# Kernel optimization log

Measured on AMD Instinct MI355X. Metric: run time of the kernel, lower is better.

## Reference

```python
import jax, jax.numpy as jnp
import numpy as np


def _hat(w):
    wx, wy, wz = w[..., 0], w[..., 1], w[..., 2]
    O = jnp.zeros_like(wx)
    return jnp.stack([
        jnp.stack([O, -wz, wy], -1),
        jnp.stack([wz, O, -wx], -1),
        jnp.stack([-wy, wx, O], -1)], -2)


def so3_exp_map(w):
    # w: [B,3] axis-angle -> [B,3,3] rotation (Rodrigues with Taylor fallback)
    th2 = jnp.sum(w * w, -1)[..., None, None]
    th = jnp.sqrt(th2 + 1e-30)
    a = jnp.where(th2 > 1e-8, jnp.sin(th) / th, 1.0 - th2 / 6.0)
    b = jnp.where(th2 > 1e-8, (1.0 - jnp.cos(th)) / th2, 0.5 - th2 / 24.0)
    K = _hat(w)
    I = jnp.eye(3, dtype=w.dtype)
    return I + a * K + b * (K @ K)


def _trilinear(vol, pts):
    # vol: [X,Y,Z]; pts: [N,3] voxel coords; zero outside the volume
    dims = jnp.asarray(vol.shape, dtype=pts.dtype)
    inside = jnp.all((pts >= 0.0) & (pts <= dims - 1.0), axis=-1)
    p0 = jnp.floor(pts)
    f = pts - p0
    hi = jnp.asarray(vol.shape, dtype=jnp.int32) - 1
    i0 = jnp.clip(p0.astype(jnp.int32), 0, hi)
    i1 = jnp.clip(i0 + 1, 0, hi)
    x0, y0, z0 = i0[:, 0], i0[:, 1], i0[:, 2]
    x1, y1, z1 = i1[:, 0], i1[:, 1], i1[:, 2]
    fx, fy, fz = f[:, 0], f[:, 1], f[:, 2]
    gx, gy, gz = 1.0 - fx, 1.0 - fy, 1.0 - fz
    val = (vol[x0, y0, z0] * gx * gy * gz + vol[x1, y0, z0] * fx * gy * gz
           + vol[x0, y1, z0] * gx * fy * gz + vol[x0, y0, z1] * gx * gy * fz
           + vol[x1, y1, z0] * fx * fy * gz + vol[x1, y0, z1] * fx * gy * fz
           + vol[x0, y1, z1] * gx * fy * fz + vol[x1, y1, z1] * fx * fy * fz)
    return jnp.where(inside, val, 0.0)


def setup_inputs() -> dict:
    key = jax.random.key(0)
    k1, k2, k3 = jax.random.split(key, 3)
    D = 256
    volume = jax.random.uniform(k1, (D, D, D), dtype=jnp.float32)
    spacing = jnp.ones(3, dtype=jnp.float32)                    # 1 mm voxels
    origin = jnp.full((3,), -(D - 1) / 2.0, dtype=jnp.float32)  # volume centered at 0
    isocenter = jnp.zeros(3, dtype=jnp.float32)
    sdd = jnp.array([1020.0], dtype=jnp.float32)
    # cam-to-world: source 510 mm behind isocenter on -z axis
    rt_inv = jnp.eye(4, dtype=jnp.float32).at[2, 3].set(-510.0)[None]
    # intrinsics: 512x512 detector, 2 mm pixels -> focal = sdd/pixel = 510
    f = 510.0
    K = jnp.array([[f, 0.0, 256.0], [0.0, f, 256.0], [0.0, 0.0, 1.0]], jnp.float32)
    k_inv = jnp.linalg.inv(K)
    eps = 1e-8
    rot = eps * jax.random.normal(k2, (1, 3), dtype=jnp.float32)
    xyz = eps * jax.random.normal(k3, (1, 3), dtype=jnp.float32)
    return {"volume": volume, "rt_inv": rt_inv, "k_inv": k_inv, "sdd": sdd,
            "isocenter": isocenter, "origin": origin, "spacing": spacing,
            "rot": rot, "xyz": xyz, "height": 512, "width": 512, "n_steps": 256}


def reference(volume, rt_inv, k_inv, sdd, isocenter, origin, spacing, rot, xyz,
              height, width, n_steps):
    dtype = volume.dtype
    # --- pose property: pivot @ exp(rot),R@xyz @ pivot_inv, then rt_inv @ pose ---
    R = so3_exp_map(rot)[0]                       # [3,3]
    t = R @ xyz[0]                                # einsum('bij,bj->bi')
    T = jnp.eye(4, dtype=dtype).at[:3, :3].set(R).at[:3, 3].set(t)
    rtm = rt_inv[0]
    c = (jnp.linalg.inv(rtm) @ jnp.append(isocenter, jnp.ones(1, dtype)))[:3]
    piv = jnp.eye(4, dtype=dtype).at[:3, 3].set(c)
    piv_inv = jnp.eye(4, dtype=dtype).at[:3, 3].set(-c)
    pose = rtm @ (piv @ (T @ piv_inv))            # cam-to-world, [4,4]
    # --- render: ray-march DRR ---
    u = jnp.arange(width, dtype=dtype) + 0.5
    v = jnp.arange(height, dtype=dtype) + 0.5
    uu, vv = jnp.meshgrid(u, v, indexing='xy')    # [H,W]
    pix = jnp.stack([uu.ravel(), vv.ravel(), jnp.ones(height * width, dtype)], -1)
    dir_cam = (pix @ k_inv.T) * sdd[0]            # detector points at depth sdd, cam frame
    Rw, src = pose[:3, :3], pose[:3, 3]
    dirs = dir_cam @ Rw.T                         # world-frame source->detector rays [N,3]
    seglen = jnp.linalg.norm(dirs, axis=-1) / n_steps

    def step(acc, i):
        frac = (i.astype(dtype) + 0.5) / n_steps
        pts = src + dirs * frac                   # [N,3] world points
        vox = (pts - origin) / spacing            # voxel coords
        return acc + _trilinear(volume, vox), None

    acc, _ = jax.lax.scan(step, jnp.zeros(height * width, dtype), jnp.arange(n_steps))
    img = acc * seglen                            # line-integral approximation
    return img.reshape(1, 1, height, width)
```

## Files before the change

### kernel.cpp

```cpp
#include <hip/hip_runtime.h>
#include <hip/hip_fp16.h>

#define W 512
#define H 512
#define NSTEPS 256
#define D 256
#define DM1 255.0f
#define QUAD_WS_BYTES (256ull*256ull*256ull*8ull)

struct SetupOut {
    float Rw[9];
    float src[3];
    float kinv[9];
    float sdd;
    float org[3];
    float invsp[3];
};

__device__ __forceinline__ void mat4mul(const float* A, const float* B, float* C) {
    #pragma unroll
    for (int i = 0; i < 4; ++i)
        #pragma unroll
        for (int j = 0; j < 4; ++j) {
            float s = 0.f;
            #pragma unroll
            for (int k = 0; k < 4; ++k) s += A[i*4+k] * B[k*4+j];
            C[i*4+j] = s;
        }
}

__device__ void compute_setup(const float* rt_inv, const float* k_inv, const float* sdd,
                              const float* isocenter, const float* origin, const float* spacing,
                              const float* rot, const float* xyz, SetupOut* o) {
    float wx = rot[0], wy = rot[1], wz = rot[2];
    float th2 = wx*wx + wy*wy + wz*wz;
    float th = sqrtf(th2 + 1e-30f);
    float a, b;
    if (th2 > 1e-8f) { a = sinf(th) / th; b = (1.f - cosf(th)) / th2; }
    else             { a = 1.f - th2 / 6.f; b = 0.5f - th2 / 24.f; }
    float K[9]  = {0.f,-wz,wy,  wz,0.f,-wx,  -wy,wx,0.f};
    float K2[9];
    #pragma unroll
    for (int i = 0; i < 3; ++i)
        #pragma unroll
        for (int j = 0; j < 3; ++j) {
            float s = 0.f;
            #pragma unroll
            for (int k = 0; k < 3; ++k) s += K[i*3+k] * K[k*3+j];
            K2[i*3+j] = s;
        }
    float R[9];
    #pragma unroll
    for (int i = 0; i < 9; ++i) R[i] = ((i % 4 == 0) ? 1.f : 0.f) + a*K[i] + b*K2[i];
    float t[3];
    #pragma unroll
    for (int i = 0; i < 3; ++i)
        t[i] = R[i*3+0]*xyz[0] + R[i*3+1]*xyz[1] + R[i*3+2]*xyz[2];

    float Ainv[16];
    const float* M = rt_inv;
    if (M[12] == 0.f && M[13] == 0.f && M[14] == 0.f && M[15] == 1.f) {
        const float r00=M[0],r01=M[1],r02=M[2],  r10=M[4],r11=M[5],r12=M[6],
                    r20=M[8],r21=M[9],r22=M[10];
        const float c00 = r11*r22 - r12*r21, c01 = r02*r21 - r01*r22, c02 = r01*r12 - r02*r11;
        const float c10 = r12*r20 - r10*r22, c11 = r00*r22 - r02*r20, c12 = r02*r10 - r00*r12;
        const float c20 = r10*r21 - r11*r20, c21 = r01*r20 - r00*r21, c22 = r00*r11 - r01*r10;
        const float det = r00*c00 + r01*c10 + r02*c20;
        const float id  = 1.f / det;
        const float tx = M[3], ty = M[7], tz = M[11];
        Ainv[0]=c00*id; Ainv[1]=c01*id; Ainv[2]=c02*id;
        Ainv[4]=c10*id; Ainv[5]=c11*id; Ainv[6]=c12*id;
        Ainv[8]=c20*id; Ainv[9]=c21*id; Ainv[10]=c22*id;
        Ainv[3]  = -(Ainv[0]*tx + Ainv[1]*ty + Ainv[2]*tz);
        Ainv[7]  = -(Ainv[4]*tx + Ainv[5]*ty + Ainv[6]*tz);
        Ainv[11] = -(Ainv[8]*tx + Ainv[9]*ty + Ainv[10]*tz);
        Ainv[12]=0.f; Ainv[13]=0.f; Ainv[14]=0.f; Ainv[15]=1.f;
    } else {
        float A[16];
        #pragma unroll
        for (int i = 0; i < 16; ++i) { A[i] = rt_inv[i]; Ainv[i] = 0.f; }
        Ainv[0] = Ainv[5] = Ainv[10] = Ainv[15] = 1.f;
        for (int c = 0; c < 4; ++c) {
            int p = c; float mx = fabsf(A[c*4+c]);
            for (int r = c+1; r < 4; ++r) { float v = fabsf(A[r*4+c]); if (v > mx) { mx = v; p = r; } }
            if (p != c) {
                for (int j = 0; j < 4; ++j) {
                    float tmp = A[c*4+j];   A[c*4+j]   = A[p*4+j];   A[p*4+j]   = tmp;
                    tmp = Ainv[c*4+j];      Ainv[c*4+j] = Ainv[p*4+j]; Ainv[p*4+j] = tmp;
                }
            }
            float inv = 1.f / A[c*4+c];
            for (int j = 0; j < 4; ++j) { A[c*4+j] *= inv; Ainv[c*4+j] *= inv; }
            for (int r = 0; r < 4; ++r) if (r != c) {
                float f = A[r*4+c];
                for (int j = 0; j < 4; ++j) { A[r*4+j] -= f*A[c*4+j]; Ainv[r*4+j] -= f*Ainv[c*4+j]; }
            }
        }
    }
    float cv[3];
    #pragma unroll
    for (int i = 0; i < 3; ++i)
        cv[i] = Ainv[i*4+0]*isocenter[0] + Ainv[i*4+1]*isocenter[1]
              + Ainv[i*4+2]*isocenter[2] + Ainv[i*4+3];

    float T[16]    = {R[0],R[1],R[2],t[0],  R[3],R[4],R[5],t[1],  R[6],R[7],R[8],t[2],  0,0,0,1};
    float piv[16]  = {1,0,0, cv[0],  0,1,0, cv[1],  0,0,1, cv[2],  0,0,0,1};
    float pivi[16] = {1,0,0,-cv[0],  0,1,0,-cv[1],  0,0,1,-cv[2],  0,0,0,1};
    float M1[16], M2[16], pose[16];
    mat4mul(T, pivi, M1);
    mat4mul(piv, M1, M2);
    mat4mul(rt_inv, M2, pose);

    #pragma unroll
    for (int i = 0; i < 3; ++i) {
        #pragma unroll
        for (int j = 0; j < 3; ++j) o->Rw[i*3+j] = pose[i*4+j];
        o->src[i] = pose[i*4+3];
    }
    #pragma unroll
    for (int i = 0; i < 9; ++i) o->kinv[i] = k_inv[i];
    o->sdd = sdd[0];
    #pragma unroll
    for (int i = 0; i < 3; ++i) { o->org[i] = origin[i]; o->invsp[i] = 1.f / spacing[i]; }
}

__global__ __launch_bounds__(256) void setup_kernel2(
    const float* __restrict__ rt_inv, const float* __restrict__ k_inv,
    const float* __restrict__ sdd, const float* __restrict__ isocenter,
    const float* __restrict__ origin, const float* __restrict__ spacing,
    const float* __restrict__ rot, const float* __restrict__ xyz,
    SetupOut* __restrict__ sp, unsigned char* __restrict__ gmask)
{
    __shared__ SetupOut S;
    if (threadIdx.x == 0) {
        compute_setup(rt_inv, k_inv, sdd, isocenter, origin, spacing, rot, xyz, &S);
        *sp = S;
    }
    __syncthreads();
    if (!gmask) return;

    __shared__ unsigned char m[256];
    m[threadIdx.x] = 0;
    __syncthreads();
    {
        const int i = threadIdx.x;
        const float frac = ((float)i + 0.5f) * (1.0f / (float)NSTEPS);
        const float Az = (S.src[2] - S.org[2]) * S.invsp[2];
        float vmin = 1e30f, vmax = -1e30f;
        #pragma unroll
        for (int c = 0; c < 4; ++c) {
            const float u = (c & 1)  ? ((float)W - 0.5f) : 0.5f;
            const float v = (c >> 1) ? ((float)H - 0.5f) : 0.5f;
            const float dcx = (S.kinv[0]*u + S.kinv[1]*v + S.kinv[2]) * S.sdd;
            const float dcy = (S.kinv[3]*u + S.kinv[4]*v + S.kinv[5]) * S.sdd;
            const float dcz = (S.kinv[6]*u + S.kinv[7]*v + S.kinv[8]) * S.sdd;
            const float dz  = S.Rw[6]*dcx + S.Rw[7]*dcy + S.Rw[8]*dcz;
            const float Bz  = dz * S.invsp[2];
            const float vz  = fmaf(Bz, frac, Az);
            vmin = fminf(vmin, vz);
            vmax = fmaxf(vmax, vz);
        }
        const int zlo = max(0,     (int)floorf(vmin - 0.05f));
        const int zhi = min(D - 1, (int)floorf(vmax + 0.05f) + 1);
        for (int z = zlo; z <= zhi; ++z) m[z] = 1;
    }
    __syncthreads();
    gmask[threadIdx.x] = m[threadIdx.x];
}

__global__ __launch_bounds__(256) void repack_quad_h(const float* __restrict__ vol,
                                                     uint2* __restrict__ ws,
                                                     const unsigned char* __restrict__ gmask) {
    const int x  = blockIdx.x;
    const int y0 = blockIdx.y * 128;
    const int z0 = blockIdx.z * 64;
    const int tid  = threadIdx.x;

    __shared__ unsigned int  tf2[129 * 32];
    __shared__ unsigned short halo_h[129];
    __shared__ unsigned char zm[64];
    const int xbase = x << 16;
    const int zh = min(z0 + 64, D - 1);

    if (tid < 64) zm[tid] = gmask ? gmask[z0 + tid] : (unsigned char)1;

    {
        const int s  = tid & 31;
        const int r0 = tid >> 5;
        for (int r = r0; r <= 128; r += 8) {
            const int y = min(y0 + r, D - 1);
            const float2 f = reinterpret_cast<const float2*>(vol + xbase + (y << 8) + z0)[s];
            __half2 h = __floats2half2_rn(f.x, f.y);
            tf2[r * 32 + (s ^ (r & 31))] = *reinterpret_cast<unsigned int*>(&h);
        }
        if (tid <= 128) {
            const int y = min(y0 + tid, D - 1);
            __half hh = __float2half_rn(vol[xbase + (y << 8) + zh]);
            halo_h[tid] = *reinterpret_cast<unsigned short*>(&hh);
        }
    }
    __syncthreads();

    const int grp  = tid >> 6;
    const int lane = tid & 63;
    const int ra = 2 * lane, rb = 2 * lane + 1, rc = 2 * lane + 2;
    for (int wp = grp; wp < 32; wp += 4) {
        const bool we = zm[2 * wp] != 0;
        const bool wo = zm[2 * wp + 1] != 0;
        if (!(we | wo)) continue;
        const unsigned int a = tf2[ra * 32 + (wp ^ (ra & 31))];
        const unsigned int b = tf2[rb * 32 + (wp ^ (rb & 31))];
        const unsigned int c = tf2[rc * 32 + (wp ^ (rc & 31))];
        const int zeven = z0 + 2 * wp;
        if (we) {
            uint4 q; q.x = a; q.y = b; q.z = b; q.w = c;
            *reinterpret_cast<uint4*>(ws + xbase + (zeven << 8) + y0 + ra) = q;
        }
        if (wo) {
            unsigned int na, nb, nc;
            if (wp < 31) {
                na = tf2[ra * 32 + ((wp + 1) ^ (ra & 31))] & 0xffffu;
                nb = tf2[rb * 32 + ((wp + 1) ^ (rb & 31))] & 0xffffu;
                nc = tf2[rc * 32 + ((wp + 1) ^ (rc & 31))] & 0xffffu;
            } else {
                na = halo_h[ra]; nb = halo_h[rb]; nc = halo_h[rc];
            }
            uint4 q;
            q.x = (a >> 16) | (na << 16);
            q.y = (b >> 16) | (nb << 16);
            q.z = q.y;
            q.w = (c >> 16) | (nc << 16);
            *reinterpret_cast<uint4*>(ws + xbase + ((zeven + 1) << 8) + y0 + ra) = q;
        }
    }
}

struct RayState {
    float Ax, Ay, Az, Bx, By, Bz, seglen;
    int imin, imax;
    bool any;
};

__device__ __forceinline__ RayState ray_setup(const SetupOut* S, int ix, int iy) {
    RayState r;
    const float u = (float)ix + 0.5f;
    const float v = (float)iy + 0.5f;
    const float dcx = (S->kinv[0]*u + S->kinv[1]*v + S->kinv[2]) * S->sdd;
    const float dcy = (S->kinv[3]*u + S->kinv[4]*v + S->kinv[5]) * S->sdd;
    const float dcz = (S->kinv[6]*u + S->kinv[7]*v + S->kinv[8]) * S->sdd;
    const float dx = S->Rw[0]*dcx + S->Rw[1]*dcy + S->Rw[2]*dcz;
    const float dy = S->Rw[3]*dcx + S->Rw[4]*dcy + S->Rw[5]*dcz;
    const float dz = S->Rw[6]*dcx + S->Rw[7]*dcy + S->Rw[8]*dcz;
    r.seglen = sqrtf(dx*dx + dy*dy + dz*dz) * (1.0f / (float)NSTEPS);
    r.Ax = (S->src[0] - S->org[0]) * S->invsp[0];
    r.Ay = (S->src[1] - S->org[1]) * S->invsp[1];
    r.Az = (S->src[2] - S->org[2]) * S->invsp[2];
    r.Bx = dx * S->invsp[0];
    r.By = dy * S->invsp[1];
    r.Bz = dz * S->invsp[2];

    float fmin = 0.f, fmax = 1.f;
    bool empty = false;
    const float aa[3] = { r.Ax, r.Ay, r.Az };
    const float bb[3] = { r.Bx, r.By, r.Bz };
    #pragma unroll
    for (int k = 0; k < 3; ++k) {
        if (fabsf(bb[k]) > 1e-12f) {
            const float rcp = 1.f / bb[k];
            const float t0 = (0.f - aa[k]) * rcp;
            const float t1 = (DM1 - aa[k]) * rcp;
            fmin = fmaxf(fmin, fminf(t0, t1));
            fmax = fminf(fmax, fmaxf(t0, t1));
        } else if (aa[k] < 0.f || aa[k] > DM1) {
            empty = true;
        }
    }
    r.any = !empty && (fmax >= fmin);
    r.imin = max(0,          (int)floorf(fmin * (float)NSTEPS - 0.5f) - 1);
    r.imax = min(NSTEPS - 1, (int)ceilf (fmax * (float)NSTEPS - 0.5f) + 1);
    return r;
}

__global__ __launch_bounds__(256) void drr_quad_kernel(
    const uint2* __restrict__ wsq, const SetupOut* __restrict__ S,
    float* __restrict__ out)
{
    const int b   = blockIdx.x;
    const int xcd = b & 7;
    const int j   = b >> 3;
    const int uu  = xcd * 16 + (j & 15);
    const int vv  = j >> 4;

    const int seg = threadIdx.x & 3;
    const int iy = vv * 16 + (threadIdx.x >> 2);
    const int ix = uu * 4  + threadIdx.y;
    const RayState r = ray_setup(S, ix, iy);

    float acc = 0.f;
    if (r.any) {
        #pragma unroll 8
        for (int i = r.imin + seg; i <= r.imax; i += 4) {
            const float frac = ((float)i + 0.5f) * (1.0f / (float)NSTEPS);
            const float vx = fmaf(r.Bx, frac, r.Ax);
            const float vy = fmaf(r.By, frac, r.Ay);
            const float vz = fmaf(r.Bz, frac, r.Az);
            const bool inside = (vx >= 0.f) && (vx <= DM1) &&
                                (vy >= 0.f) && (vy <= DM1) &&
                                (vz >= 0.f) && (vz <= DM1);
            const float cx = fminf(fmaxf(vx, 0.f), DM1);
            const float cy = fminf(fmaxf(vy, 0.f), DM1);
            const float cz = fminf(fmaxf(vz, 0.f), DM1);
            const float px = floorf(cx), py = floorf(cy), pz = floorf(cz);
            const int x0 = (int)px, y0 = (int)py, z0 = (int)pz;
            const int x1 = min(x0 + 1, D - 1);
            const float fx = cx - px, fy = cy - py, fz = cz - pz;
            const float gx = 1.f - fx, gy = 1.f - fy, gz = 1.f - fz;

            const int e0 = (x0 << 16) + (z0 << 8) + y0;
            const int e1 = e0 + ((x1 - x0) << 16);

            const uint2 q0 = wsq[e0];
            const uint2 q1 = wsq[e1];
            const float2 a0 = __half22float2(*reinterpret_cast<const __half2*>(&q0.x));
            const float2 a1 = __half22float2(*reinterpret_cast<const __half2*>(&q0.y));
            const float2 b0 = __half22float2(*reinterpret_cast<const __half2*>(&q1.x));
            const float2 b1 = __half22float2(*reinterpret_cast<const __half2*>(&q1.y));

            const float c00 = a0.x*gz + a0.y*fz;
            const float c01 = a1.x*gz + a1.y*fz;
            const float c10 = b0.x*gz + b0.y*fz;
            const float c11 = b1.x*gz + b1.y*fz;
            const float samp = (c00*gy + c01*fy)*gx + (c10*gy + c11*fy)*fx;
            acc += inside ? samp : 0.f;
        }
    }
    acc += __shfl_xor(acc, 1);
    acc += __shfl_xor(acc, 2);
    if (seg == 0)
        out[iy * W + ix] = acc * r.seglen;
}

__global__ __launch_bounds__(256) void drr_direct_kernel(
    const float* __restrict__ vol,
    const float* __restrict__ rt_inv, const float* __restrict__ k_inv,
    const float* __restrict__ sdd, const float* __restrict__ isocenter,
    const float* __restrict__ origin, const float* __restrict__ spacing,
    const float* __restrict__ rot, const float* __restrict__ xyz,
    float* __restrict__ out)
{
    __shared__ SetupOut S;
    if (threadIdx.x == 0 && threadIdx.y == 0)
        compute_setup(rt_inv, k_inv, sdd, isocenter, origin, spacing, rot, xyz, &S);
    __syncthreads();

    const int seg = threadIdx.x & 1;
    const int iy = blockIdx.x * 32 + (threadIdx.x >> 1);
    const int ix = blockIdx.y * 4  + threadIdx.y;
    const RayState r = ray_setup(&S, ix, iy);

    float acc = 0.f;
    if (r.any) {
        #pragma unroll 4
        for (int i = r.imin + seg; i <= r.imax; i += 2) {
            const float frac = ((float)i + 0.5f) * (1.0f / (float)NSTEPS);
            const float vx = fmaf(r.Bx, frac, r.Ax);
            const float vy = fmaf(r.By, frac, r.Ay);
            const float vz = fmaf(r.Bz, frac, r.Az);
            const bool inside = (vx >= 0.f) && (vx <= DM1) &&
                                (vy >= 0.f) && (vy <= DM1) &&
                                (vz >= 0.f) && (vz <= DM1);
            const float cx = fminf(fmaxf(vx, 0.f), DM1);
            const float cy = fminf(fmaxf(vy, 0.f), DM1);
            const float cz = fminf(fmaxf(vz, 0.f), DM1);
            const float px = floorf(cx), py = floorf(cy), pz = floorf(cz);
            const int x0 = (int)px, y0 = (int)py, z0 = (int)pz;
            const int x1 = min(x0 + 1, D - 1);
            const int y1 = min(y0 + 1, D - 1);
            const int z1 = min(z0 + 1, D - 1);
            const float fx = cx - px, fy = cy - py, fz = cz - pz;
            const float gx = 1.f - fx, gy = 1.f - fy, gz = 1.f - fz;

            const int base = (x0 << 16) + (y0 << 8);
            const int bx = (x1 - x0) << 16;
            const int by = (y1 - y0) << 8;

            const float v000 = vol[base + z0],           v001 = vol[base + z1];
            const float v010 = vol[base + by + z0],      v011 = vol[base + by + z1];
            const float v100 = vol[base + bx + z0],      v101 = vol[base + bx + z1];
            const float v110 = vol[base + bx + by + z0], v111 = vol[base + bx + by + z1];

            const float c00 = v000*gz + v001*fz;
            const float c01 = v010*gz + v011*fz;
            const float c10 = v100*gz + v101*fz;
            const float c11 = v110*gz + v111*fz;
            const float samp = (c00*gy + c01*fy)*gx + (c10*gy + c11*fy)*fx;
            acc += inside ? samp : 0.f;
        }
    }
    acc += __shfl_xor(acc, 1);
    if (seg == 0)
        out[iy * W + ix] = acc * r.seglen;
}

extern "C" void kernel_launch(void* const* d_in, const int* in_sizes, int n_in,
                              void* d_out, int out_size, void* d_ws, size_t ws_size,
                              hipStream_t stream) {
    const float* vol      = (const float*)d_in[0];
    const float* rt_inv   = (const float*)d_in[1];
    const float* k_inv    = (const float*)d_in[2];
    const float* sdd      = (const float*)d_in[3];
    const float* iso      = (const float*)d_in[4];
    const float* origin   = (const float*)d_in[5];
    const float* spacing  = (const float*)d_in[6];
    const float* rot      = (const float*)d_in[7];
    const float* xyz      = (const float*)d_in[8];
    float* out = (float*)d_out;

    if (ws_size >= QUAD_WS_BYTES + 4096) {
        uint2* wsq = (uint2*)d_ws;
        SetupOut* sp = (SetupOut*)((char*)d_ws + QUAD_WS_BYTES);
        unsigned char* gmask = (unsigned char*)d_ws + QUAD_WS_BYTES + 512;

        setup_kernel2<<<1, 256, 0, stream>>>(rt_inv, k_inv, sdd, iso, origin,
                                             spacing, rot, xyz, sp, gmask);
        repack_quad_h<<<dim3(D, 2, 4), 256, 0, stream>>>(vol, wsq, gmask);
        drr_quad_kernel<<<dim3(4096), dim3(64, 4), 0, stream>>>(wsq, sp, out);
    } else if (ws_size >= QUAD_WS_BYTES) {
        uint2* wsq = (uint2*)d_ws;
        SetupOut* sp = (SetupOut*)((char*)d_ws + (QUAD_WS_BYTES - 128));

        repack_quad_h<<<dim3(D, 2, 4), 256, 0, stream>>>(vol, wsq, nullptr);
        setup_kernel2<<<1, 256, 0, stream>>>(rt_inv, k_inv, sdd, iso, origin,
                                             spacing, rot, xyz, sp, nullptr);
        drr_quad_kernel<<<dim3(4096), dim3(64, 4), 0, stream>>>(wsq, sp, out);
    } else {
        drr_direct_kernel<<<dim3(H / 32, W / 4), dim3(64, 4), 0, stream>>>(
            vol, rt_inv, k_inv, sdd, iso, origin, spacing, rot, xyz, out);
    }
}
```

Before: 61.50 us.

## Replace quad-packed fp16 volume with y-pair packing to halve workspace

Changes the repacked fp16 workspace so each entry stores a y-neighbour pair (4 bytes) instead of a 2x2 y/z quad (8 bytes). This halves the repack write traffic and the workspace footprint. The cost is that the ray-march kernel now issues four gathers per sample instead of two. It also removes the fallback path used when the workspace is smaller and lowers the loop unroll from 8 to 4.

```diff
diff --git a/kernel.cpp b/kernel.cpp
--- a/kernel.cpp
+++ b/kernel.cpp
@@ -6,7 +6,7 @@
 #define NSTEPS 256
 #define D 256
 #define DM1 255.0f
-#define QUAD_WS_BYTES (256ull*256ull*256ull*8ull)
+#define PAIR_WS_BYTES (256ull*256ull*256ull*4ull)
 
 struct SetupOut {
     float Rw[9];
@@ -168,19 +168,17 @@
     gmask[threadIdx.x] = m[threadIdx.x];
 }
 
-__global__ __launch_bounds__(256) void repack_quad_h(const float* __restrict__ vol,
-                                                     uint2* __restrict__ ws,
+__global__ __launch_bounds__(256) void repack_pair_t(const float* __restrict__ vol,
+                                                     unsigned int* __restrict__ ws,
                                                      const unsigned char* __restrict__ gmask) {
     const int x  = blockIdx.x;
     const int y0 = blockIdx.y * 128;
     const int z0 = blockIdx.z * 64;
     const int tid  = threadIdx.x;
 
-    __shared__ unsigned int  tf2[129 * 32];
-    __shared__ unsigned short halo_h[129];
+    __shared__ unsigned int tf2[129 * 32];
     __shared__ unsigned char zm[64];
     const int xbase = x << 16;
-    const int zh = min(z0 + 64, D - 1);
 
     if (tid < 64) zm[tid] = gmask ? gmask[z0 + tid] : (unsigned char)1;
 
@@ -193,45 +191,23 @@
             __half2 h = __floats2half2_rn(f.x, f.y);
             tf2[r * 32 + (s ^ (r & 31))] = *reinterpret_cast<unsigned int*>(&h);
         }
-        if (tid <= 128) {
-            const int y = min(y0 + tid, D - 1);
-            __half hh = __float2half_rn(vol[xbase + (y << 8) + zh]);
-            halo_h[tid] = *reinterpret_cast<unsigned short*>(&hh);
-        }
     }
     __syncthreads();
 
     const int grp  = tid >> 6;
     const int lane = tid & 63;
     const int ra = 2 * lane, rb = 2 * lane + 1, rc = 2 * lane + 2;
-    for (int wp = grp; wp < 32; wp += 4) {
-        const bool we = zm[2 * wp] != 0;
-        const bool wo = zm[2 * wp + 1] != 0;
-        if (!(we | wo)) continue;
-        const unsigned int a = tf2[ra * 32 + (wp ^ (ra & 31))];
-        const unsigned int b = tf2[rb * 32 + (wp ^ (rb & 31))];
-        const unsigned int c = tf2[rc * 32 + (wp ^ (rc & 31))];
-        const int zeven = z0 + 2 * wp;
-        if (we) {
-            uint4 q; q.x = a; q.y = b; q.z = b; q.w = c;
-            *reinterpret_cast<uint4*>(ws + xbase + (zeven << 8) + y0 + ra) = q;
-        }
-        if (wo) {
-            unsigned int na, nb, nc;
-            if (wp < 31) {
-                na = tf2[ra * 32 + ((wp + 1) ^ (ra & 31))] & 0xffffu;
-                nb = tf2[rb * 32 + ((wp + 1) ^ (rb & 31))] & 0xffffu;
-                nc = tf2[rc * 32 + ((wp + 1) ^ (rc & 31))] & 0xffffu;
-            } else {
-                na = halo_h[ra]; nb = halo_h[rb]; nc = halo_h[rc];
-            }
-            uint4 q;
-            q.x = (a >> 16) | (na << 16);
-            q.y = (b >> 16) | (nb << 16);
-            q.z = q.y;
-            q.w = (c >> 16) | (nc << 16);
-            *reinterpret_cast<uint4*>(ws + xbase + ((zeven + 1) << 8) + y0 + ra) = q;
-        }
+    for (int w = grp; w < 64; w += 4) {
+        if (!zm[w]) continue;
+        const int wp = w >> 1;
+        const int sh = (w & 1) << 4;
+        const unsigned int ha = (tf2[ra * 32 + (wp ^ (ra & 31))] >> sh) & 0xffffu;
+        const unsigned int hb = (tf2[rb * 32 + (wp ^ (rb & 31))] >> sh) & 0xffffu;
+        const unsigned int hc = (tf2[rc * 32 + (wp ^ (rc & 31))] >> sh) & 0xffffu;
+        uint2 q;
+        q.x = ha | (hb << 16);
+        q.y = hb | (hc << 16);
+        *reinterpret_cast<uint2*>(ws + xbase + ((z0 + w) << 8) + y0 + ra) = q;
     }
 }
 
@@ -281,8 +257,8 @@
     return r;
 }
 
-__global__ __launch_bounds__(256) void drr_quad_kernel(
-    const uint2* __restrict__ wsq, const SetupOut* __restrict__ S,
+__global__ __launch_bounds__(256) void drr_pair_kernel(
+    const unsigned int* __restrict__ wsp, const SetupOut* __restrict__ S,
     float* __restrict__ out)
 {
     const int b   = blockIdx.x;
@@ -298,7 +274,7 @@
 
     float acc = 0.f;
     if (r.any) {
-        #pragma unroll 8
+        #pragma unroll 4
         for (int i = r.imin + seg; i <= r.imax; i += 4) {
             const float frac = ((float)i + 0.5f) * (1.0f / (float)NSTEPS);
             const float vx = fmaf(r.Bx, frac, r.Ax);
@@ -313,24 +289,31 @@
             const float px = floorf(cx), py = floorf(cy), pz = floorf(cz);
             const int x0 = (int)px, y0 = (int)py, z0 = (int)pz;
             const int x1 = min(x0 + 1, D - 1);
+            const int z1 = min(z0 + 1, D - 1);
             const float fx = cx - px, fy = cy - py, fz = cz - pz;
             const float gx = 1.f - fx, gy = 1.f - fy, gz = 1.f - fz;
 
-            const int e0 = (x0 << 16) + (z0 << 8) + y0;
-            const int e1 = e0 + ((x1 - x0) << 16);
-
-            const uint2 q0 = wsq[e0];
-            const uint2 q1 = wsq[e1];
-            const float2 a0 = __half22float2(*reinterpret_cast<const __half2*>(&q0.x));
-            const float2 a1 = __half22float2(*reinterpret_cast<const __half2*>(&q0.y));
-            const float2 b0 = __half22float2(*reinterpret_cast<const __half2*>(&q1.x));
-            const float2 b1 = __half22float2(*reinterpret_cast<const __half2*>(&q1.y));
-
-            const float c00 = a0.x*gz + a0.y*fz;
-            const float c01 = a1.x*gz + a1.y*fz;
-            const float c10 = b0.x*gz + b0.y*fz;
-            const float c11 = b1.x*gz + b1.y*fz;
-            const float samp = (c00*gy + c01*fy)*gx + (c10*gy + c11*fy)*fx;
+            const int e00 = (x0 << 16) + (z0 << 8) + y0;
+            const int zo  = (z1 - z0) << 8;
+            const int xo  = (x1 - x0) << 16;
+
+            const unsigned int q00 = wsp[e00];
+            const unsigned int q01 = wsp[e00 + zo];
+            const unsigned int q10 = wsp[e00 + xo];
+            const unsigned int q11 = wsp[e00 + xo + zo];
+
+            const float2 a00 = __half22float2(*reinterpret_cast<const __half2*>(&q00));
+            const float2 a01 = __half22float2(*reinterpret_cast<const __half2*>(&q01));
+            const float2 a10 = __half22float2(*reinterpret_cast<const __half2*>(&q10));
+            const float2 a11 = __half22float2(*reinterpret_cast<const __half2*>(&q11));
+
+            const float m00 = a00.x*gy + a00.y*fy;
+            const float m01 = a01.x*gy + a01.y*fy;
+            const float m10 = a10.x*gy + a10.y*fy;
+            const float m11 = a11.x*gy + a11.y*fy;
+            const float c0 = m00*gz + m01*fz;
+            const float c1 = m10*gz + m11*fz;
+            const float samp = c0*gx + c1*fx;
             acc += inside ? samp : 0.f;
         }
     }
@@ -416,23 +399,15 @@
     const float* xyz      = (const float*)d_in[8];
     float* out = (float*)d_out;
 
-    if (ws_size >= QUAD_WS_BYTES + 4096) {
-        uint2* wsq = (uint2*)d_ws;
-        SetupOut* sp = (SetupOut*)((char*)d_ws + QUAD_WS_BYTES);
-        unsigned char* gmask = (unsigned char*)d_ws + QUAD_WS_BYTES + 512;
+    if (ws_size >= PAIR_WS_BYTES + 4096) {
+        unsigned int* wsp = (unsigned int*)d_ws;
+        SetupOut* sp = (SetupOut*)((char*)d_ws + PAIR_WS_BYTES);
+        unsigned char* gmask = (unsigned char*)d_ws + PAIR_WS_BYTES + 512;
 
         setup_kernel2<<<1, 256, 0, stream>>>(rt_inv, k_inv, sdd, iso, origin,
                                              spacing, rot, xyz, sp, gmask);
-        repack_quad_h<<<dim3(D, 2, 4), 256, 0, stream>>>(vol, wsq, gmask);
-        drr_quad_kernel<<<dim3(4096), dim3(64, 4), 0, stream>>>(wsq, sp, out);
-    } else if (ws_size >= QUAD_WS_BYTES) {
-        uint2* wsq = (uint2*)d_ws;
-        SetupOut* sp = (SetupOut*)((char*)d_ws + (QUAD_WS_BYTES - 128));
-
-        repack_quad_h<<<dim3(D, 2, 4), 256, 0, stream>>>(vol, wsq, nullptr);
-        setup_kernel2<<<1, 256, 0, stream>>>(rt_inv, k_inv, sdd, iso, origin,
-                                             spacing, rot, xyz, sp, nullptr);
-        drr_quad_kernel<<<dim3(4096), dim3(64, 4), 0, stream>>>(wsq, sp, out);
+        repack_pair_t<<<dim3(D, 2, 4), 256, 0, stream>>>(vol, wsp, gmask);
+        drr_pair_kernel<<<dim3(4096), dim3(64, 4), 0, stream>>>(wsp, sp, out);
     } else {
         drr_direct_kernel<<<dim3(H / 32, W / 4), dim3(64, 4), 0, stream>>>(
             vol, rt_inv, k_inv, sdd, iso, origin, spacing, rot, xyz, out);
```

New measurement: 53.49 us. -13.0%, faster.
